# Performance work log

Measured on AMD Instinct MI355X. Metric: run time of the kernel, lower is better.

## Reference

```python
import jax, jax.numpy as jnp
import numpy as np

B, T, F, H, TL = 256, 512, 64, 1024, 64

def _gru_step(h, x, W_ih, W_hh, b_ih, b_hh):
    # torch nn.GRU cell semantics
    gi = x @ W_ih.T + b_ih          # [B, 3H]
    gh = h @ W_hh.T + b_hh          # [B, 3H]
    ir, iz, inn = jnp.split(gi, 3, axis=-1)
    hr, hz, hn = jnp.split(gh, 3, axis=-1)
    r = jax.nn.sigmoid(ir + hr)
    z = jax.nn.sigmoid(iz + hz)
    n = jnp.tanh(inn + r * hn)
    return (1.0 - z) * n + z * h

def setup_inputs() -> dict:
    key = jax.random.key(0)
    ks = jax.random.split(key, 12)
    s_e = 1.0 / np.sqrt(H)
    u = lambda k, shp: jax.random.uniform(k, shp, jnp.float32, -s_e, s_e)
    return {
        "x": jax.random.normal(ks[0], (B, T, F), jnp.float32),
        "enc_W_ih": u(ks[1], (3 * H, F)),
        "enc_W_hh": u(ks[2], (3 * H, H)),
        "enc_b_ih": u(ks[3], (3 * H,)),
        "enc_b_hh": u(ks[4], (3 * H,)),
        "dec_W_ih": u(ks[5], (3 * H, 1)),
        "dec_W_hh": u(ks[6], (3 * H, H)),
        "dec_b_ih": u(ks[7], (3 * H,)),
        "dec_b_hh": u(ks[8], (3 * H,)),
        "fc_W": u(ks[9], (1, H)),
        "fc_b": u(ks[10], (1,)),
    }

def reference(x, enc_W_ih, enc_W_hh, enc_b_ih, enc_b_hh,
              dec_W_ih, dec_W_hh, dec_b_ih, dec_b_hh, fc_W, fc_b):
    b = x.shape[0]
    h0 = jnp.zeros((b, H), x.dtype)

    # encoder: sequential GRU over time
    def enc_step(h, xt):
        return _gru_step(h, xt, enc_W_ih, enc_W_hh, enc_b_ih, enc_b_hh), None
    h_enc, _ = jax.lax.scan(enc_step, h0, jnp.swapaxes(x, 0, 1))  # [B, H]

    inp0 = jnp.zeros((b, 1), x.dtype)
    def dec_step(carry, _):
        h, inp = carry
        h = _gru_step(h, inp, dec_W_ih, dec_W_hh, dec_b_ih, dec_b_hh)
        out = h @ fc_W.T + fc_b  # [B, 1]
        return (h, out), out
    _, outs = jax.lax.scan(dec_step, (h_enc, inp0), None, length=TL)  # [TL, B, 1]
    return jnp.swapaxes(outs, 0, 1)  # [B, TL, 1]
```

## Files before the change

kernel.cpp:

```cpp
#include <hip/hip_runtime.h>

#define B_  256
#define T_  512
#define F_  64
#define H_  1024
#define TL_ 64

typedef _Float16 half8 __attribute__((ext_vector_type(8)));
typedef float   floatx4 __attribute__((ext_vector_type(4)));
typedef unsigned long long ull;

#define MFMA(a, b, c) __builtin_amdgcn_mfma_f32_16x16x32_f16(a, b, c, 0, 0, 0)

#define WF_E   0UL
#define WF_D   6291456UL
#define WF_I   12582912UL
#define HP     12976128UL
#define PSTR   524288UL
#define PB     15073280UL
#define BARS   15204352UL

__device__ __forceinline__ void sta8(void* p, ull v) {
  __hip_atomic_store((ull*)p, v, __ATOMIC_RELAXED, __HIP_MEMORY_SCOPE_AGENT);
}
__device__ __forceinline__ float lda4f(const float* p) {
  return __hip_atomic_load(p, __ATOMIC_RELAXED, __HIP_MEMORY_SCOPE_AGENT);
}

__global__ void gru_setup(const float* __restrict__ WhhE,
                          const float* __restrict__ WhhD,
                          const float* __restrict__ WihE,
                          char* __restrict__ ws) {
  int t = blockIdx.x * 256 + threadIdx.x;
  if (t < 512) ((unsigned int*)(ws + BARS))[t] = 0u;
  const int NW = 3 * 64 * 32 * 4 * 16;
  if (t < 2 * NW) {
    const float* W = (t < NW) ? WhhE : WhhD;
    size_t dst = (t < NW) ? WF_E : WF_D;
    int c = (t < NW) ? t : t - NW;
    int r = c & 15, q = (c >> 4) & 3, kb = (c >> 6) & 31, gj = c >> 11;
    int row = (gj >> 6) * H_ + (gj & 63) * 16 + r;
    const float* src = W + (size_t)row * H_ + kb * 32 + q * 8;
    half8 v;
#pragma unroll
    for (int i = 0; i < 8; ++i) v[i] = (_Float16)src[i];
    *(half8*)(ws + dst + (size_t)c * 16) = v;
  } else if (t < 2 * NW + 3 * 64 * 2 * 4 * 16) {
    int c = t - 2 * NW;
    int r = c & 15, q = (c >> 4) & 3, kc = (c >> 6) & 1, gj = c >> 7;
    int row = (gj >> 6) * H_ + (gj & 63) * 16 + r;
    const float* src = WihE + (size_t)row * F_ + kc * 32 + q * 8;
    half8 v;
#pragma unroll
    for (int i = 0; i < 8; ++i) v[i] = (_Float16)src[i];
    *(half8*)(ws + WF_I + (size_t)c * 16) = v;
  }
}

__device__ __forceinline__ void gbar(unsigned int* cnt, unsigned int target) {
  __syncthreads();
  if (threadIdx.x == 0) {
    __hip_atomic_fetch_add(cnt, 1u, __ATOMIC_RELAXED,
                           __HIP_MEMORY_SCOPE_AGENT);
    while (__hip_atomic_load(cnt, __ATOMIC_RELAXED,
                             __HIP_MEMORY_SCOPE_AGENT) < target)
      __builtin_amdgcn_s_sleep(1);
  }
  __syncthreads();
}

__global__ __launch_bounds__(512, 2) void gru_main(
    const float* __restrict__ x,
    const float* __restrict__ bih_e, const float* __restrict__ bhh_e,
    const float* __restrict__ Wih_d,
    const float* __restrict__ bih_d, const float* __restrict__ bhh_d,
    const float* __restrict__ fcW, const float* __restrict__ fcb,
    float* __restrict__ out, char* __restrict__ ws) {

  __shared__ __align__(128) char atile[32768];
  __shared__ float red[4 * 64 * 17];
  __shared__ __align__(16) char otile[2048];
  __shared__ float inp_lds[16];

  const int tid = threadIdx.x;
  const int L = tid & 63;
  const int w = tid >> 6;
  const int jp = w & 3;
  const int kh = w >> 2;
  const int bx = blockIdx.x;
  const int rg = bx & 15;
  const int cb = bx >> 4;
  const int r = L & 15;
  const int q = L >> 4;
  const int jg = cb * 4 + jp;
  const int jc = jg * 16 + r;

  unsigned int* bar = (unsigned int*)(ws + BARS) + (size_t)rg * 32;
  unsigned int bt = 0;

  const size_t slab = (size_t)rg * 32768;

  if (tid < 256) {
    sta8(ws + HP + slab + (size_t)cb * 2048 + (size_t)tid * 8, 0ull);
  }

  float hold[4] = {0.f, 0.f, 0.f, 0.f};
  const float fcb_s = *fcb;
  const float fcw_l = fcW[jc];

  bt += 16;
  gbar(bar, bt);

  for (int phase = 0; phase < 2; ++phase) {
    half8 bW[48];
    {
      const char* wf = ws + (phase ? WF_D : WF_E);
#pragma unroll
      for (int g = 0; g < 3; ++g)
#pragma unroll
        for (int kk = 0; kk < 16; ++kk)
          bW[g * 16 + kk] = *(const half8*)(
              wf + (size_t)((g * 64 + jg) * 32 + kh * 16 + kk) * 1024 +
              (size_t)L * 16);
#pragma unroll
      for (int i = 0; i < 48; ++i) asm volatile("" : "+v"(bW[i]));
    }
    const float* bih = phase ? bih_d : bih_e;
    const float* bhh = phase ? bhh_d : bhh_e;
    const float b_r  = bih[jc]          + bhh[jc];
    const float b_z  = bih[H_ + jc]     + bhh[H_ + jc];
    const float b_in = bih[2 * H_ + jc];
    const float b_hn = bhh[2 * H_ + jc];
    float wd_r = 0.f, wd_z = 0.f, wd_n = 0.f;
    if (phase) {
      wd_r = Wih_d[jc]; wd_z = Wih_d[H_ + jc]; wd_n = Wih_d[2 * H_ + jc];
    }

    const int nsteps = phase ? TL_ : T_;
    for (int d = 0; d < nsteps; ++d) {
      const int s = phase ? T_ + d : d;

      {
        const char* srcbase = ws + HP + (size_t)(s & 1) * PSTR + slab;
#pragma unroll
        for (int c = 0; c < 4; ++c) {
          const int seg = w * 4 + c;
          const char* src = srcbase + (size_t)seg * 1024 + (size_t)L * 16;
          __builtin_amdgcn_global_load_lds(
              (const __attribute__((address_space(1))) void*)src,
              (__attribute__((address_space(3))) void*)(atile + seg * 1024),
              16, 0, 17);
        }
      }

      if (phase && tid < 16) {
        float sum = 0.f;
        if (d > 0) {
          const float* pb =
              (const float*)(ws + PB) + (size_t)((d + 1) & 1) * 64 * 256;
          int row = rg * 16 + tid;
          float a = fcb_s;
          for (int jj = 0; jj < 64; ++jj) a += lda4f(&pb[jj * 256 + row]);
          sum = a;
          if (cb == 0) out[(size_t)row * TL_ + (d - 1)] = a;
        }
        inp_lds[tid] = sum;
      }
      __syncthreads();

      floatx4 a0 = {0.f, 0.f, 0.f, 0.f}, a1 = {0.f, 0.f, 0.f, 0.f};
      floatx4 a2 = {0.f, 0.f, 0.f, 0.f}, aI = {0.f, 0.f, 0.f, 0.f};

#pragma unroll
      for (int kk = 0; kk < 16; ++kk) {
        const int kb = kh * 16 + kk;
        half8 ahi = *(const half8*)(atile + kb * 1024 + L * 16);
        a0 = MFMA(ahi, bW[kk], a0);
        a1 = MFMA(ahi, bW[16 + kk], a1);
        a2 = MFMA(ahi, bW[32 + kk], a2);
      }

      if (kh == 1) {
        if (!phase) {
          const float* xp =
              x + ((size_t)(rg * 16 + r) * T_ + s) * F_ + q * 8;
          const char* wfi = ws + WF_I + (size_t)L * 16;
#pragma unroll
          for (int kc = 0; kc < 2; ++kc) {
            floatx4 x0 = *(const floatx4*)(xp + kc * 32);
            floatx4 x1 = *(const floatx4*)(xp + kc * 32 + 4);
            half8 xa;
#pragma unroll
            for (int i = 0; i < 4; ++i) {
              xa[i] = (_Float16)x0[i];
              xa[4 + i] = (_Float16)x1[i];
            }
            a0 = MFMA(xa, *(const half8*)(wfi +
                     (size_t)((0 * 64 + jg) * 2 + kc) * 1024), a0);
            a1 = MFMA(xa, *(const half8*)(wfi +
                     (size_t)((1 * 64 + jg) * 2 + kc) * 1024), a1);
            aI = MFMA(xa, *(const half8*)(wfi +
                     (size_t)((2 * 64 + jg) * 2 + kc) * 1024), aI);
          }
        }
        float* rd = &red[(jp * 64 + L) * 17];
#pragma unroll
        for (int i = 0; i < 4; ++i) {
          rd[i] = a0[i];
          rd[4 + i] = a1[i];
          rd[8 + i] = a2[i];
        }
        if (!phase) {
#pragma unroll
          for (int i = 0; i < 4; ++i) rd[12 + i] = aI[i];
        }
      }
      __syncthreads();

      if (kh == 0) {
        const float* rd = &red[(jp * 64 + L) * 17];
        const size_t tbase = (size_t)(jp >> 1) * 1024 +
                             (size_t)((jp & 1) * 2 + (r >> 3)) * 256 +
                             (size_t)(r & 7) * 2;
        float pv[4];
#pragma unroll
        for (int i = 0; i < 4; ++i) {
          float rpre = a0[i] + rd[i] + b_r;
          float zpre = a1[i] + rd[4 + i] + b_z;
          float hn   = a2[i] + rd[8 + i] + b_hn;
          float inn  = b_in + (phase ? 0.f : rd[12 + i]);
          if (phase) {
            float inp = inp_lds[q * 4 + i];
            rpre += inp * wd_r;
            zpre += inp * wd_z;
            inn  += inp * wd_n;
          }
          float rg_ = 1.f / (1.f + __expf(-rpre));
          float zg = 1.f / (1.f + __expf(-zpre));
          float t2 = __expf(-2.f * (inn + rg_ * hn));
          float ng = 2.f / (1.f + t2) - 1.f;
          float hnew = (1.f - zg) * ng + zg * hold[i];
          hold[i] = hnew;
          *(_Float16*)(otile + tbase + (size_t)(q * 4 + i) * 16) =
              (_Float16)hnew;
          pv[i] = hnew * fcw_l;
        }
        if (phase) {
#pragma unroll
          for (int i = 0; i < 4; ++i) {
            float v = pv[i];
            v += __shfl_xor(v, 1);
            v += __shfl_xor(v, 2);
            v += __shfl_xor(v, 4);
            v += __shfl_xor(v, 8);
            if (r == 0) {
              float* pb = (float*)(ws + PB) + (size_t)(d & 1) * 64 * 256;
              __hip_atomic_store(&pb[jg * 256 + (rg * 16 + q * 4 + i)], v,
                                 __ATOMIC_RELAXED, __HIP_MEMORY_SCOPE_AGENT);
            }
          }
        }
      }
      __syncthreads();

      if (tid < 256) {
        ull v = *(const ull*)(otile + (size_t)tid * 8);
        sta8(ws + HP + (size_t)((s + 1) & 1) * PSTR + slab +
                 (size_t)cb * 2048 + (size_t)tid * 8,
             v);
      }

      bt += 16;
      gbar(bar, bt);
    }
  }

  if (cb == 0 && tid < 16) {
    const float* pb =
        (const float*)(ws + PB) + (size_t)((TL_ - 1) & 1) * 64 * 256;
    int row = rg * 16 + tid;
    float a = fcb_s;
    for (int jj = 0; jj < 64; ++jj) a += lda4f(&pb[jj * 256 + row]);
    out[(size_t)row * TL_ + (TL_ - 1)] = a;
  }
}

extern "C" void kernel_launch(void* const* d_in, const int* in_sizes, int n_in,
                              void* d_out, int out_size, void* d_ws,
                              size_t ws_size, hipStream_t stream) {
  const float* x     = (const float*)d_in[0];
  const float* WihE  = (const float*)d_in[1];
  const float* WhhE  = (const float*)d_in[2];
  const float* bihE  = (const float*)d_in[3];
  const float* bhhE  = (const float*)d_in[4];
  const float* WihD  = (const float*)d_in[5];
  const float* WhhD  = (const float*)d_in[6];
  const float* bihD  = (const float*)d_in[7];
  const float* bhhD  = (const float*)d_in[8];
  const float* fcW   = (const float*)d_in[9];
  const float* fcb   = (const float*)d_in[10];
  float* outp = (float*)d_out;
  char* ws = (char*)d_ws;

  gru_setup<<<3168, 256, 0, stream>>>(WhhE, WhhD, WihE, ws);

  gru_main<<<dim3(256), dim3(512), 0, stream>>>(
      x, bihE, bhhE, WihD, bihD, bhhD, fcW, fcb, outp, ws);
}
```

Before: 2.736 ms.

## Map row groups to XCCs so hidden-state exchange stays within one L2

```diff
diff --git a/kernel.cpp b/kernel.cpp
--- a/kernel.cpp
+++ b/kernel.cpp
@@ -24,6 +24,9 @@
   __hip_atomic_store((ull*)p, v, __ATOMIC_RELAXED, __HIP_MEMORY_SCOPE_AGENT);
 }
 __device__ __forceinline__ float lda4f(const float* p) {
+  return __hip_atomic_load(p, __ATOMIC_RELAXED, __HIP_MEMORY_SCOPE_AGENT);
+}
+__device__ __forceinline__ unsigned lda4u(const unsigned* p) {
   return __hip_atomic_load(p, __ATOMIC_RELAXED, __HIP_MEMORY_SCOPE_AGENT);
 }
 
@@ -81,6 +84,8 @@
   __shared__ float red[4 * 64 * 17];
   __shared__ __align__(16) char otile[2048];
   __shared__ float inp_lds[16];
+  __shared__ unsigned char xmap[256];
+  __shared__ int disc[3];
 
   const int tid = threadIdx.x;
   const int L = tid & 63;
@@ -88,10 +93,54 @@
   const int jp = w & 3;
   const int kh = w >> 2;
   const int bx = blockIdx.x;
-  const int rg = bx & 15;
-  const int cb = bx >> 4;
   const int r = L & 15;
   const int q = L >> 4;
+
+  {
+    unsigned* map = (unsigned*)(ws + PB);
+    unsigned* dbar = (unsigned*)(ws + BARS) + 1;
+    if (tid == 0) {
+      unsigned xcc;
+      asm volatile("s_getreg_b32 %0, hwreg(HW_REG_XCC_ID)" : "=s"(xcc));
+      __hip_atomic_store(map + bx, xcc & 15u, __ATOMIC_RELAXED,
+                         __HIP_MEMORY_SCOPE_AGENT);
+    }
+    __syncthreads();
+    if (tid == 0) {
+      __hip_atomic_fetch_add(dbar, 1u, __ATOMIC_RELAXED,
+                             __HIP_MEMORY_SCOPE_AGENT);
+      while (lda4u(dbar) < 256u) __builtin_amdgcn_s_sleep(1);
+    }
+    __syncthreads();
+    if (tid < 256) xmap[tid] = (unsigned char)(lda4u(map + tid) & 255u);
+    __syncthreads();
+    if (tid == 0) {
+      int cnt[8] = {0, 0, 0, 0, 0, 0, 0, 0};
+      int myx = xmap[bx], rank = 0, ok = 1;
+      for (int i = 0; i < 256; ++i) {
+        int xi = xmap[i];
+        if (xi > 7) { ok = 0; break; }
+        cnt[xi]++;
+        if (i < bx && xi == myx) rank++;
+      }
+      if (ok)
+        for (int i = 0; i < 8; ++i) ok &= (cnt[i] == 32);
+      if (ok) {
+        disc[0] = myx * 2 + (rank >> 4);
+        disc[1] = rank & 15;
+        disc[2] = 1;
+      } else {
+        disc[0] = bx & 15;
+        disc[1] = bx >> 4;
+        disc[2] = 0;
+      }
+    }
+    __syncthreads();
+  }
+  const int rg = disc[0];
+  const int cb = disc[1];
+  const int loc = disc[2];
+
   const int jg = cb * 4 + jp;
   const int jc = jg * 16 + r;
 
@@ -142,14 +191,26 @@
 
       {
         const char* srcbase = ws + HP + (size_t)(s & 1) * PSTR + slab;
-#pragma unroll
-        for (int c = 0; c < 4; ++c) {
-          const int seg = w * 4 + c;
-          const char* src = srcbase + (size_t)seg * 1024 + (size_t)L * 16;
-          __builtin_amdgcn_global_load_lds(
-              (const __attribute__((address_space(1))) void*)src,
-              (__attribute__((address_space(3))) void*)(atile + seg * 1024),
-              16, 0, 17);
+        if (loc) {
+#pragma unroll
+          for (int c = 0; c < 4; ++c) {
+            const int seg = w * 4 + c;
+            const char* src = srcbase + (size_t)seg * 1024 + (size_t)L * 16;
+            __builtin_amdgcn_global_load_lds(
+                (const __attribute__((address_space(1))) void*)src,
+                (__attribute__((address_space(3))) void*)(atile + seg * 1024),
+                16, 0, 1);
+          }
+        } else {
+#pragma unroll
+          for (int c = 0; c < 4; ++c) {
+            const int seg = w * 4 + c;
+            const char* src = srcbase + (size_t)seg * 1024 + (size_t)L * 16;
+            __builtin_amdgcn_global_load_lds(
+                (const __attribute__((address_space(1))) void*)src,
+                (__attribute__((address_space(3))) void*)(atile + seg * 1024),
+                16, 0, 17);
+          }
         }
       }
 
@@ -265,9 +326,13 @@
 
       if (tid < 256) {
         ull v = *(const ull*)(otile + (size_t)tid * 8);
-        sta8(ws + HP + (size_t)((s + 1) & 1) * PSTR + slab +
-                 (size_t)cb * 2048 + (size_t)tid * 8,
-             v);
+        char* p = ws + HP + (size_t)((s + 1) & 1) * PSTR + slab +
+                  (size_t)cb * 2048 + (size_t)tid * 8;
+        if (loc) {
+          *(volatile ull*)p = v;
+        } else {
+          sta8(p, v);
+        }
       }
 
       bt += 16;
```

New measurement: 3.989 ms. 45.8% more time.

## Replace per-step group barrier with per-producer step flags and local tile copy

Applied to the files above, without the earlier changes.

```diff
diff --git a/kernel.cpp b/kernel.cpp
--- a/kernel.cpp
+++ b/kernel.cpp
@@ -23,7 +23,13 @@
 __device__ __forceinline__ void sta8(void* p, ull v) {
   __hip_atomic_store((ull*)p, v, __ATOMIC_RELAXED, __HIP_MEMORY_SCOPE_AGENT);
 }
+__device__ __forceinline__ void sta4(unsigned* p, unsigned v) {
+  __hip_atomic_store(p, v, __ATOMIC_RELAXED, __HIP_MEMORY_SCOPE_AGENT);
+}
 __device__ __forceinline__ float lda4f(const float* p) {
+  return __hip_atomic_load(p, __ATOMIC_RELAXED, __HIP_MEMORY_SCOPE_AGENT);
+}
+__device__ __forceinline__ unsigned lda4u(const unsigned* p) {
   return __hip_atomic_load(p, __ATOMIC_RELAXED, __HIP_MEMORY_SCOPE_AGENT);
 }
 
@@ -95,12 +101,13 @@
   const int jg = cb * 4 + jp;
   const int jc = jg * 16 + r;
 
-  unsigned int* bar = (unsigned int*)(ws + BARS) + (size_t)rg * 32;
-  unsigned int bt = 0;
+  unsigned int* line = (unsigned int*)(ws + BARS) + (size_t)rg * 32;
+  unsigned int* tgs = line + 8;
 
   const size_t slab = (size_t)rg * 32768;
 
   if (tid < 256) {
+    *(ull*)(otile + (size_t)tid * 8) = 0ull;
     sta8(ws + HP + slab + (size_t)cb * 2048 + (size_t)tid * 8, 0ull);
   }
 
@@ -108,8 +115,7 @@
   const float fcb_s = *fcb;
   const float fcw_l = fcW[jc];
 
-  bt += 16;
-  gbar(bar, bt);
+  gbar(line, 16);
 
   for (int phase = 0; phase < 2; ++phase) {
     half8 bW[48];
@@ -139,23 +145,41 @@
     const int nsteps = phase ? TL_ : T_;
     for (int d = 0; d < nsteps; ++d) {
       const int s = phase ? T_ + d : d;
+      const unsigned gate = (unsigned)s;
 
       {
         const char* srcbase = ws + HP + (size_t)(s & 1) * PSTR + slab;
 #pragma unroll
-        for (int c = 0; c < 4; ++c) {
-          const int seg = w * 4 + c;
-          const char* src = srcbase + (size_t)seg * 1024 + (size_t)L * 16;
-          __builtin_amdgcn_global_load_lds(
-              (const __attribute__((address_space(1))) void*)src,
-              (__attribute__((address_space(3))) void*)(atile + seg * 1024),
-              16, 0, 17);
+        for (int c = 0; c < 2; ++c) {
+          const int j = w * 2 + c;
+          if (j == cb) {
+#pragma unroll
+            for (int t2 = 0; t2 < 2; ++t2)
+              *(half8*)(atile + (size_t)(j * 2 + t2) * 1024 +
+                        (size_t)L * 16) =
+                  *(const half8*)(otile + (size_t)t2 * 1024 +
+                                  (size_t)L * 16);
+          } else {
+            while (lda4u(tgs + j) < gate) __builtin_amdgcn_s_sleep(1);
+#pragma unroll
+            for (int t2 = 0; t2 < 2; ++t2) {
+              const int seg = j * 2 + t2;
+              const char* src =
+                  srcbase + (size_t)seg * 1024 + (size_t)L * 16;
+              __builtin_amdgcn_global_load_lds(
+                  (const __attribute__((address_space(1))) void*)src,
+                  (__attribute__((address_space(3))) void*)(atile +
+                                                           seg * 1024),
+                  16, 0, 17);
+            }
+          }
         }
       }
 
       if (phase && tid < 16) {
         float sum = 0.f;
         if (d > 0) {
+          while (lda4u(tgs + tid) < gate) __builtin_amdgcn_s_sleep(1);
           const float* pb =
               (const float*)(ws + PB) + (size_t)((d + 1) & 1) * 64 * 256;
           int row = rg * 16 + tid;
@@ -269,13 +293,14 @@
                  (size_t)cb * 2048 + (size_t)tid * 8,
              v);
       }
-
-      bt += 16;
-      gbar(bar, bt);
+      __syncthreads();
+      if (tid == 0) sta4(tgs + cb, (unsigned)(s + 1));
     }
   }
 
   if (cb == 0 && tid < 16) {
+    while (lda4u(tgs + tid) < (unsigned)(T_ + TL_))
+      __builtin_amdgcn_s_sleep(1);
     const float* pb =
         (const float*)(ws + PB) + (size_t)((TL_ - 1) & 1) * 64 * 256;
     int row = rg * 16 + tid;
```

Measured after the change: 3.994 ms. 46.0% more time.

## Replace counter grid barrier with per-block step tags and hoist input MFMAs

Applied to the files above, without the earlier changes.

```diff
diff --git a/kernel.cpp b/kernel.cpp
--- a/kernel.cpp
+++ b/kernel.cpp
@@ -23,7 +23,13 @@
 __device__ __forceinline__ void sta8(void* p, ull v) {
   __hip_atomic_store((ull*)p, v, __ATOMIC_RELAXED, __HIP_MEMORY_SCOPE_AGENT);
 }
+__device__ __forceinline__ void sta4(unsigned* p, unsigned v) {
+  __hip_atomic_store(p, v, __ATOMIC_RELAXED, __HIP_MEMORY_SCOPE_AGENT);
+}
 __device__ __forceinline__ float lda4f(const float* p) {
+  return __hip_atomic_load(p, __ATOMIC_RELAXED, __HIP_MEMORY_SCOPE_AGENT);
+}
+__device__ __forceinline__ unsigned lda4u(const unsigned* p) {
   return __hip_atomic_load(p, __ATOMIC_RELAXED, __HIP_MEMORY_SCOPE_AGENT);
 }
 
@@ -95,8 +101,8 @@
   const int jg = cb * 4 + jp;
   const int jc = jg * 16 + r;
 
-  unsigned int* bar = (unsigned int*)(ws + BARS) + (size_t)rg * 32;
-  unsigned int bt = 0;
+  unsigned int* line = (unsigned int*)(ws + BARS) + (size_t)rg * 32;
+  unsigned int* tgs = line + 8;
 
   const size_t slab = (size_t)rg * 32768;
 
@@ -108,8 +114,7 @@
   const float fcb_s = *fcb;
   const float fcw_l = fcW[jc];
 
-  bt += 16;
-  gbar(bar, bt);
+  gbar(line, 16);
 
   for (int phase = 0; phase < 2; ++phase) {
     half8 bW[48];
@@ -136,9 +141,12 @@
       wd_r = Wih_d[jc]; wd_z = Wih_d[H_ + jc]; wd_n = Wih_d[2 * H_ + jc];
     }
 
+    const char* wfi = ws + WF_I + (size_t)L * 16;
+
     const int nsteps = phase ? TL_ : T_;
     for (int d = 0; d < nsteps; ++d) {
       const int s = phase ? T_ + d : d;
+      const unsigned tnext = (unsigned)(s + 1);
 
       {
         const char* srcbase = ws + HP + (size_t)(s & 1) * PSTR + slab;
@@ -153,6 +161,28 @@
         }
       }
 
+      floatx4 a0 = {0.f, 0.f, 0.f, 0.f}, a1 = {0.f, 0.f, 0.f, 0.f};
+      floatx4 aI = {0.f, 0.f, 0.f, 0.f};
+      if (!phase && kh == 1) {
+        const float* xp = x + ((size_t)(rg * 16 + r) * T_ + s) * F_ + q * 8;
+#pragma unroll
+        for (int kc = 0; kc < 2; ++kc) {
+          floatx4 x0 = *(const floatx4*)(xp + kc * 32);
+          floatx4 x1 = *(const floatx4*)(xp + kc * 32 + 4);
+          half8 xa;
+#pragma unroll
+          for (int i = 0; i < 4; ++i) {
+            xa[i] = (_Float16)x0[i];
+            xa[4 + i] = (_Float16)x1[i];
+          }
+          a0 = MFMA(xa, *(const half8*)(wfi +
+                   (size_t)((0 * 64 + jg) * 2 + kc) * 1024), a0);
+          a1 = MFMA(xa, *(const half8*)(wfi +
+                   (size_t)((1 * 64 + jg) * 2 + kc) * 1024), a1);
+          aI = MFMA(xa, *(const half8*)(wfi +
+                   (size_t)((2 * 64 + jg) * 2 + kc) * 1024), aI);
+        }
+      }
       if (phase && tid < 16) {
         float sum = 0.f;
         if (d > 0) {
@@ -168,8 +198,7 @@
       }
       __syncthreads();
 
-      floatx4 a0 = {0.f, 0.f, 0.f, 0.f}, a1 = {0.f, 0.f, 0.f, 0.f};
-      floatx4 a2 = {0.f, 0.f, 0.f, 0.f}, aI = {0.f, 0.f, 0.f, 0.f};
+      floatx4 a2 = {0.f, 0.f, 0.f, 0.f};
 
 #pragma unroll
       for (int kk = 0; kk < 16; ++kk) {
@@ -181,28 +210,6 @@
       }
 
       if (kh == 1) {
-        if (!phase) {
-          const float* xp =
-              x + ((size_t)(rg * 16 + r) * T_ + s) * F_ + q * 8;
-          const char* wfi = ws + WF_I + (size_t)L * 16;
-#pragma unroll
-          for (int kc = 0; kc < 2; ++kc) {
-            floatx4 x0 = *(const floatx4*)(xp + kc * 32);
-            floatx4 x1 = *(const floatx4*)(xp + kc * 32 + 4);
-            half8 xa;
-#pragma unroll
-            for (int i = 0; i < 4; ++i) {
-              xa[i] = (_Float16)x0[i];
-              xa[4 + i] = (_Float16)x1[i];
-            }
-            a0 = MFMA(xa, *(const half8*)(wfi +
-                     (size_t)((0 * 64 + jg) * 2 + kc) * 1024), a0);
-            a1 = MFMA(xa, *(const half8*)(wfi +
-                     (size_t)((1 * 64 + jg) * 2 + kc) * 1024), a1);
-            aI = MFMA(xa, *(const half8*)(wfi +
-                     (size_t)((2 * 64 + jg) * 2 + kc) * 1024), aI);
-          }
-        }
         float* rd = &red[(jp * 64 + L) * 17];
 #pragma unroll
         for (int i = 0; i < 4; ++i) {
@@ -260,18 +267,22 @@
             }
           }
         }
-      }
+        ull v8 = *(const ull*)(otile + (size_t)jp * 512 + (size_t)L * 8);
+        sta8(ws + HP + (size_t)((s + 1) & 1) * PSTR + slab +
+                 (size_t)cb * 2048 + (size_t)jp * 512 + (size_t)L * 8,
+             v8);
+      }
+
       __syncthreads();
-
-      if (tid < 256) {
-        ull v = *(const ull*)(otile + (size_t)tid * 8);
-        sta8(ws + HP + (size_t)((s + 1) & 1) * PSTR + slab +
-                 (size_t)cb * 2048 + (size_t)tid * 8,
-             v);
-      }
-
-      bt += 16;
-      gbar(bar, bt);
+      if (tid == 0) sta4(tgs + cb, tnext);
+      if (w == 0) {
+        for (;;) {
+          unsigned tag = (L < 16) ? lda4u(tgs + L) : tnext;
+          if (__all((int)(tag >= tnext))) break;
+          __builtin_amdgcn_s_sleep(1);
+        }
+      }
+      __syncthreads();
     }
   }
 
```

Result: faster. 2.607 ms, median of 2 (-4.7%).
